# Optimization experiments

Hardware: AMD Instinct MI355X
Metric: run time of the kernel (lower is better)

The kernel has to match this reference:

```python
import jax, jax.numpy as jnp
import numpy as np

TOP_K = 48
NUM_RBF = 16
NUM_RBF_SC = 8
MAXREL = 32
EDGE_F = 128
EPS_D = 1e-6
LN_EPS = 1e-5


def gather_nodes(nodes, idx):
    # nodes: [B, L, C], idx: [B, L, K] -> [B, L, K, C]
    return jax.vmap(lambda n, i: n[i])(nodes, idx)


def rbf(D, count):
    # D: [..., ] -> [..., count]; mu in [2, 22], sigma = 20/count
    mu = jnp.linspace(2.0, 22.0, count)
    sigma = (22.0 - 2.0) / count
    return jnp.exp(-(((D[..., None] - mu) / sigma) ** 2))


def layer_norm(x, g, b):
    mu = jnp.mean(x, -1, keepdims=True)
    var = jnp.mean((x - mu) ** 2, -1, keepdims=True)
    return g * (x - mu) / jnp.sqrt(var + LN_EPS) + b


def setup_inputs() -> dict:
    key = jax.random.key(0)
    ks = jax.random.split(key, 8)
    B, Lr = 1, 1024
    X = jax.random.normal(ks[0], (B, Lr, 37, 3), dtype=jnp.float32)
    mask = jnp.ones((B, Lr), dtype=jnp.float32)
    atom_mask = jnp.ones((B, Lr, 37), dtype=jnp.float32)
    residue_idx = jnp.arange(B * Lr, dtype=jnp.int64 if jax.config.jax_enable_x64 else jnp.int32).reshape(B, Lr)
    dihedral_mask = jnp.ones((B, Lr), dtype=jnp.float32)
    chain_labels = jnp.zeros((B, Lr), dtype=jnp.int32)
    W_pos = jax.random.normal(ks[1], (16, 2 * MAXREL + 2), dtype=jnp.float32) * 0.1
    b_pos = jnp.zeros((16,), dtype=jnp.float32)
    W_e = jax.random.normal(ks[2], (EDGE_F, 16 + NUM_RBF * 25), dtype=jnp.float32) * 0.05
    g_e = jnp.ones((EDGE_F,), dtype=jnp.float32)
    be_e = jnp.zeros((EDGE_F,), dtype=jnp.float32)
    W_s = jax.random.normal(ks[3], (EDGE_F, NUM_RBF_SC * 32 * 5), dtype=jnp.float32) * 0.05
    g_s = jnp.ones((EDGE_F,), dtype=jnp.float32)
    b_s = jnp.zeros((EDGE_F,), dtype=jnp.float32)
    return {"X": X, "L": 1024, "mask": mask, "atom_mask": atom_mask,
            "residue_idx": residue_idx, "dihedral_mask": dihedral_mask,
            "chain_labels": chain_labels, "W_pos": W_pos, "b_pos": b_pos,
            "W_e": W_e, "g_e": g_e, "be_e": be_e, "W_s": W_s, "g_s": g_s, "b_s": b_s}


def reference(X, L, mask, atom_mask, residue_idx, dihedral_mask, chain_labels,
              W_pos, b_pos, W_e, g_e, be_e, W_s, g_s, b_s):
    # Virtual Cb from ideal geometry
    b_v = X[:, :, 1, :] - X[:, :, 0, :]
    c_v = X[:, :, 2, :] - X[:, :, 1, :]
    a_v = jnp.cross(b_v, c_v)
    Cb = -0.58273431 * a_v + 0.56802827 * b_v - 0.54067466 * c_v + X[:, :, 1, :]
    Ca = X[:, :, 1, :]
    N = X[:, :, 0, :]
    C = X[:, :, 2, :]
    O = X[:, :, 4, :]

    # _dist: masked pairwise Ca distances + top-k smallest
    mask2d = mask[:, None, :] * mask[:, :, None]  # [B, L, L]
    dX = Ca[:, :, None, :] - Ca[:, None, :, :]
    D = mask2d * jnp.sqrt(jnp.sum(dX ** 2, -1) + EPS_D)
    D_max = jnp.max(D, -1, keepdims=True)
    D_adj = D + (1.0 - mask2d) * D_max
    neg_vals, E_idx = jax.lax.top_k(-D_adj, TOP_K)
    D_neighbors = -neg_vals  # [B, L, K]

    coords = {'N': N, 'Ca': Ca, 'C': C, 'O': O, 'Cb': Cb}
    pairs = [('N','N'),('C','C'),('O','O'),('Cb','Cb'),('Ca','N'),('Ca','C'),('Ca','O'),
             ('Ca','Cb'),('N','C'),('N','O'),('N','Cb'),('Cb','C'),('Cb','O'),('O','C'),
             ('N','Ca'),('C','Ca'),('O','Ca'),('Cb','Ca'),('C','N'),('O','N'),('Cb','N'),
             ('C','Cb'),('O','Cb'),('C','O')]
    A_st = jnp.stack([coords[a] for a, _ in pairs])  # [24, B, L, 3]
    B_st = jnp.stack([coords[b] for _, b in pairs])
    B_nb = jax.vmap(gather_nodes, (0, None))(B_st, E_idx)  # [24, B, L, K, 3]
    Dp = jnp.sqrt(jnp.sum((A_st[:, :, :, None, :] - B_nb) ** 2, -1) + EPS_D)  # [24,B,L,K]
    RBF_pairs = rbf(Dp, NUM_RBF)  # [24, B, L, K, 16]
    Bt, Lr, K = E_idx.shape
    RBF_pairs = jnp.moveaxis(RBF_pairs, 0, 3).reshape(Bt, Lr, K, 24 * NUM_RBF)
    RBF_all = jnp.concatenate([rbf(D_neighbors, NUM_RBF), RBF_pairs], -1)  # [B,L,K,400]

    # Positional encodings
    ri_nb = gather_nodes(residue_idx[..., None], E_idx)[..., 0]  # [B,L,K]
    offset = residue_idx[:, :, None] - ri_nb
    ch_nb = gather_nodes(chain_labels[..., None], E_idx)[..., 0]
    E_chains = (chain_labels[:, :, None] - ch_nb == 0).astype(jnp.int32)
    d = jnp.clip(offset + MAXREL, 0, 2 * MAXREL) * E_chains + (1 - E_chains) * (2 * MAXREL + 1)
    d_onehot = jax.nn.one_hot(d, 2 * MAXREL + 2, dtype=jnp.float32)
    E_positional = d_onehot @ W_pos.T + b_pos
    E = jnp.concatenate([E_positional, RBF_all], -1)  # [B,L,K,416]

    # Sidechain RBFs on the first min(100, K) neighbors
    Ks = min(100, K)
    E_idx_sub = E_idx[:, :, :Ks]
    am_g = gather_nodes(atom_mask, E_idx_sub)  # [B,L,Ks,37]
    S = X[:, :, 5:37, :]  # [B,L,32,3]
    S_nb = gather_nodes(S.reshape(Bt, Lr, 32 * 3), E_idx_sub).reshape(Bt, Lr, Ks, 32, 3)
    anchors = jnp.stack([N, Ca, C, O, Cb], 2)  # [B,L,5,3], anchor order matches loop order
    Ds = jnp.sqrt(jnp.sum((anchors[:, :, None, :, None, :] - S_nb[:, :, :, None, :, :]) ** 2, -1) + EPS_D)
    # Ds: [B,L,Ks,5,32]; rbf_side -> [B,L,Ks,5,32,8]; masked by neighbor atom mask
    RBF_s = rbf(Ds, NUM_RBF_SC) * am_g[:, :, :, None, 5:37, None]
    E_s = RBF_s.reshape(Bt, Lr, Ks, 5 * 32 * NUM_RBF_SC)  # [B,L,Ks,1280]

    E_s = layer_norm(E_s @ W_s.T, g_s, b_s)
    E = layer_norm(E @ W_e.T, g_e, be_e)
    return (E, E_idx, E_s, E_idx_sub)
```

## Files before the change

### kernel.cpp

```cpp
#include <hip/hip_runtime.h>
#include <math.h>

#define LRES 1024
#define TOPK 48
#define NEDGE (LRES*TOPK)

typedef short short8 __attribute__((ext_vector_type(8)));
typedef float f32x4  __attribute__((ext_vector_type(4)));

#define OUT_E     0
#define OUT_EIDX  6291456
#define OUT_ES    6340608
#define OUT_EIDX2 12632064

#define WS_COORDS 0
#define WS_DNB    15360
#define WS_EIDX   64512
#define WS_WPE    113664
#define WS_WPS    140288

#define DE 1.06666667f
#define QE 0.10273976f
#define DS 1.14285714f
#define QS 0.07337053f

__constant__ int PA[24] = {0,2,3,4,1,1,1,1,0,0,0,4,4,3,0,2,3,4,2,3,4,2,3,2};
__constant__ int PB[24] = {0,2,3,4,0,2,3,4,2,3,4,2,3,2,1,1,1,1,0,0,0,4,4,3};

__device__ inline short f2bf(float f) {
    unsigned u = __float_as_uint(f);
    unsigned r = (u + 0x7FFFu + ((u >> 16) & 1u)) >> 16;
    return (short)r;
}

__device__ inline short8 pack8(const float* fv) {
    union { short8 s; unsigned u[4]; } r;
    #pragma unroll
    for (int i = 0; i < 4; ++i)
        r.u[i] = __builtin_amdgcn_perm(__float_as_uint(fv[2*i+1]),
                                       __float_as_uint(fv[2*i]), 0x07060302u);
    return r.s;
}

__device__ __forceinline__ void kred_ln(const f32x4 (*acc)[8], float* hb,
                                        float* outp, const float* g,
                                        const float* b, int t, int w,
                                        int quad, int l16) {
    int e = t >> 4, c = t & 15;
    float gv[8], bv[8];
    #pragma unroll
    for (int k = 0; k < 8; ++k) { gv[k] = g[c + 16*k]; bv[k] = b[c + 16*k]; }
    float* hw = hb + w*2144;
    #pragma unroll
    for (int mt = 0; mt < 2; ++mt) {
        __syncthreads();
        #pragma unroll
        for (int nt = 0; nt < 8; ++nt)
        #pragma unroll
        for (int r = 0; r < 4; ++r)
            hw[(quad*4 + r)*134 + nt*16 + l16] = acc[mt][nt][r];
        __syncthreads();
        float s = 0.f, s2 = 0.f, vals[8];
        #pragma unroll
        for (int k = 0; k < 8; ++k) {
            int col = e*134 + c + 16*k;
            float v = hb[col] + hb[2144 + col] + hb[4288 + col] + hb[6432 + col];
            vals[k] = v; s += v; s2 = fmaf(v, v, s2);
        }
        #pragma unroll
        for (int m = 1; m <= 8; m <<= 1) {
            s  += __shfl_xor(s,  m);
            s2 += __shfl_xor(s2, m);
        }
        float mu = s * 0.0078125f;
        float rs = rsqrtf(fmaf(s2, 0.0078125f, -mu*mu) + 1e-5f);
        float* row = outp + (size_t)(mt*16 + e)*128 + c;
        #pragma unroll
        for (int k = 0; k < 8; ++k)
            __builtin_nontemporal_store(gv[k]*(vals[k] - mu)*rs + bv[k],
                                        &row[16*k]);
    }
}

__global__ __launch_bounds__(256) void k_pre(const float* __restrict__ X,
                                             const float* __restrict__ mask,
                                             const float* __restrict__ We,
                                             const float* __restrict__ Ws,
                                             float* __restrict__ coords,
                                             short* __restrict__ WpE,
                                             short* __restrict__ WpS,
                                             float* __restrict__ Dnb,
                                             int* __restrict__ Eidx,
                                             float* __restrict__ out) {
    int blk = blockIdx.x, t = threadIdx.x;
    if (blk < 256) {
        __shared__ float sCa[LRES*3];
        __shared__ float sM[LRES];
        for (int j = t; j < LRES; j += 256) {
            sCa[j*3+0] = X[j*111 + 3];
            sCa[j*3+1] = X[j*111 + 4];
            sCa[j*3+2] = X[j*111 + 5];
            sM[j] = mask[j];
        }
        __syncthreads();
        int w = t >> 6, lane = t & 63;
        int i = blk * 4 + w;
        float cx = sCa[i*3], cy = sCa[i*3+1], cz = sCa[i*3+2];
        float mi = sM[i];
        float dv[16], m2v[16];
        float lmax = -1e30f;
        #pragma unroll
        for (int s = 0; s < 16; ++s) {
            int j = s*64 + lane;
            float dx = cx - sCa[j*3], dy = cy - sCa[j*3+1], dz = cz - sCa[j*3+2];
            float d  = __builtin_amdgcn_sqrtf(dx*dx + dy*dy + dz*dz + 1e-6f);
            float m2 = mi * sM[j];
            dv[s] = m2 * d; m2v[s] = m2;
            lmax = fmaxf(lmax, dv[s]);
        }
        #pragma unroll
        for (int off = 32; off; off >>= 1) lmax = fmaxf(lmax, __shfl_xor(lmax, off));
        unsigned long long key[16];
        unsigned long long mkey = ~0ull; int mslot = 0;
        #pragma unroll
        for (int s = 0; s < 16; ++s) {
            float dadj = dv[s] + (1.0f - m2v[s]) * lmax;
            key[s] = (((unsigned long long)__float_as_uint(dadj)) << 10) | (unsigned)(s*64 + lane);
            if (key[s] < mkey) { mkey = key[s]; mslot = s; }
        }
        for (int it = 0; it < TOPK; ++it) {
            unsigned long long wk = mkey;
            #pragma unroll
            for (int off = 32; off; off >>= 1) {
                unsigned long long o = __shfl_xor(wk, off);
                wk = (o < wk) ? o : wk;
            }
            if (lane == 0) {
                int j = (int)(wk & 1023u);
                int id = i*TOPK + it;
                Dnb[id]  = __uint_as_float((unsigned)(wk >> 10));
                Eidx[id] = j;
                out[OUT_EIDX  + id] = (float)j;
                out[OUT_EIDX2 + id] = (float)j;
            }
            if (mkey == wk) {
                key[mslot] = ~0ull;
                mkey = ~0ull;
                #pragma unroll
                for (int s = 0; s < 16; ++s)
                    if (key[s] < mkey) { mkey = key[s]; mslot = s; }
            }
        }
    } else if (blk < 896) {
        int g = (blk - 256) * 256 + t;
        if (g < 8*13*64*8) {
            int j = g & 7, lane = (g >> 3) & 63, gg = g >> 9;
            int ks = gg % 13, nt = gg / 13;
            int n = nt*16 + (lane & 15), k = ks*32 + (lane >> 4)*8 + j;
            WpE[g] = f2bf(We[n*416 + k]);
        }
        if (g < 8*40*64*8) {
            int j = g & 7, lane = (g >> 3) & 63, gg = g >> 9;
            int ks = gg % 40, nt = gg / 40;
            int n = nt*16 + (lane & 15), k = ks*32 + (lane >> 4)*8 + j;
            WpS[g] = f2bf(Ws[n*1280 + k]);
        }
    } else {
        int r = (blk - 896) * 256 + t;
        if (r >= LRES) return;
        const float* xr = X + r * 111;
        float N[3], Ca[3], C[3], O[3], bv[3], cv[3], av[3];
        #pragma unroll
        for (int d = 0; d < 3; ++d) {
            N[d]  = xr[0*3 + d];  Ca[d] = xr[1*3 + d];
            C[d]  = xr[2*3 + d];  O[d]  = xr[4*3 + d];
            bv[d] = Ca[d] - N[d]; cv[d] = C[d] - Ca[d];
        }
        av[0] = bv[1]*cv[2] - bv[2]*cv[1];
        av[1] = bv[2]*cv[0] - bv[0]*cv[2];
        av[2] = bv[0]*cv[1] - bv[1]*cv[0];
        float* o = coords + r * 15;
        #pragma unroll
        for (int d = 0; d < 3; ++d) {
            float Cb = -0.58273431f*av[d] + 0.56802827f*bv[d] - 0.54067466f*cv[d] + Ca[d];
            o[0*3+d] = N[d]; o[1*3+d] = Ca[d]; o[2*3+d] = C[d];
            o[3*3+d] = O[d]; o[4*3+d] = Cb;
        }
    }
}

__global__ __launch_bounds__(256, 2) void k_edge(const float* __restrict__ coords,
                                                 const float* __restrict__ X,
                                                 const float* __restrict__ amask,
                                                 const short* __restrict__ WpE,
                                                 const short* __restrict__ WpS,
                                                 const float* __restrict__ Dnb,
                                                 const int* __restrict__ Eidx,
                                                 const int* __restrict__ ri,
                                                 const int* __restrict__ ch,
                                                 const float* __restrict__ Wpos,
                                                 const float* __restrict__ bpos,
                                                 const float* __restrict__ ge,
                                                 const float* __restrict__ be,
                                                 const float* __restrict__ gs,
                                                 const float* __restrict__ bs,
                                                 float* __restrict__ out) {
    __shared__ float smem[9536];
    int t = threadIdx.x;
    int w = t >> 6, lane = t & 63, quad = lane >> 4, l16 = lane & 15;
    float* hb = smem;

    if (blockIdx.x < 1536) {
        float* sA3 = smem + 8576;
        int id0 = blockIdx.x * 32;
        int i0 = id0 / TOPK;

        if (t < 45) {
            int rr = i0 + t / 15;
            if (rr > LRES-1) rr = LRES-1;
            sA3[t] = coords[rr*15 + t%15];
        }
        int s1 = 4*w + quad;
        float S[2][2][3], am[2][2];
        int im[2];
        #pragma unroll
        for (int mt = 0; mt < 2; ++mt) {
            int id = id0 + mt*16 + l16;
            int j  = Eidx[id];
            im[mt] = id / TOPK;
            const float* xp = X + (j*37 + 5)*3;
            const float* ap = amask + j*37 + 5;
            #pragma unroll
            for (int h = 0; h < 2; ++h) {
                int s = s1 + h*16;
                S[mt][h][0] = xp[s*3+0];
                S[mt][h][1] = xp[s*3+1];
                S[mt][h][2] = xp[s*3+2];
                am[mt][h]   = ap[s];
            }
        }
        __syncthreads();

        f32x4 acc[2][8] = {};
        const short8* bp = (const short8*)WpS;

        for (int a = 0; a < 5; ++a) {
            float A[2][3];
            #pragma unroll
            for (int mt = 0; mt < 2; ++mt) {
                int base = (im[mt] - i0)*15 + a*3;
                A[mt][0] = sA3[base+0];
                A[mt][1] = sA3[base+1];
                A[mt][2] = sA3[base+2];
            }
            #pragma unroll
            for (int h = 0; h < 2; ++h) {
                int ks = a*8 + w + h*4;
                short8 afrag[2];
                #pragma unroll
                for (int mt = 0; mt < 2; ++mt) {
                    float dx = A[mt][0] - S[mt][h][0];
                    float dy = A[mt][1] - S[mt][h][1];
                    float dz = A[mt][2] - S[mt][h][2];
                    float d  = __builtin_amdgcn_sqrtf(fmaf(dz,dz,fmaf(dy,dy,fmaf(dx,dx,1e-6f))));
                    float u  = fmaf(d, 0.4f, -0.8f);
                    float e0 = __expf(-u*u) * am[mt][h];
                    float g  = __expf(fmaf(2.0f*DS, u, -DS*DS));
                    float fv[8];
                    fv[0] = e0;
                    #pragma unroll
                    for (int r = 1; r < 8; ++r) { e0 *= g; g *= QS; fv[r] = e0; }
                    afrag[mt] = pack8(fv);
                }
                #pragma unroll
                for (int nt = 0; nt < 8; ++nt) {
                    short8 b = bp[(nt*40 + ks)*64 + lane];
                    acc[0][nt] = __builtin_amdgcn_mfma_f32_16x16x32_bf16(afrag[0], b, acc[0][nt], 0,0,0);
                    acc[1][nt] = __builtin_amdgcn_mfma_f32_16x16x32_bf16(afrag[1], b, acc[1][nt], 0,0,0);
                }
            }
        }
        kred_ln(acc, hb, out + OUT_ES + (size_t)id0*128, gs, bs, t, w, quad, l16);
    } else {
        float* sA    = smem + 8576;
        float* sB    = smem + 9056;
        float* sdist = hb;
        float* sposf = hb + 864;
        int*   sdpos = (int*)(hb + 1408);
        int id0 = (blockIdx.x - 1536) * 32;

        if (t < 32) {
            int id = id0 + t, i = id / TOPK, j = Eidx[id];
            int off = ri[i] - ri[j];
            sdpos[t] = (ch[i] == ch[j]) ? min(max(off + 32, 0), 64) : 65;
            sdist[t*27] = Dnb[id];
        }
        for (int it = t; it < 32*15; it += 256) {
            int e = it / 15, q = it % 15;
            int id = id0 + e, i = id / TOPK, j = Eidx[id];
            sA[e*15+q] = coords[i*15+q];
            sB[e*15+q] = coords[j*15+q];
        }
        __syncthreads();
        for (int it = t; it < 32*24; it += 256) {
            int e = it / 24, p = it % 24, a = PA[p], b = PB[p];
            float dx = sA[e*15+a*3+0] - sB[e*15+b*3+0];
            float dy = sA[e*15+a*3+1] - sB[e*15+b*3+1];
            float dz = sA[e*15+a*3+2] - sB[e*15+b*3+2];
            sdist[e*27 + 1 + p] = __builtin_amdgcn_sqrtf(dx*dx + dy*dy + dz*dz + 1e-6f);
        }
        for (int it = t; it < 32*16; it += 256) {
            int e = it >> 4, c = it & 15;
            sposf[e*17 + c] = Wpos[c*66 + sdpos[e]] + bpos[c];
        }
        __syncthreads();

        f32x4 acc[2][8] = {};
        const short8* bp = (const short8*)WpE;
        float rb = (quad & 1) ? 8.0f*DE : 0.0f;

        for (int ks = w; ks < 13; ks += 4) {
            short8 afrag[2];
            #pragma unroll
            for (int mt = 0; mt < 2; ++mt) {
                int e = mt*16 + l16;
                float fv[8];
                if (ks == 0 && quad < 2) {
                    #pragma unroll
                    for (int j = 0; j < 8; ++j) fv[j] = sposf[e*17 + quad*8 + j];
                } else {
                    int p = (ks == 0) ? 0 : (2*ks - 1 + (quad >> 1));
                    float d = sdist[e*27 + p];
                    float u = fmaf(d, 0.8f, -1.6f) - rb;
                    float e0 = __expf(-u*u);
                    float g  = __expf(fmaf(2.0f*DE, u, -DE*DE));
                    fv[0] = e0;
                    #pragma unroll
                    for (int r = 1; r < 8; ++r) { e0 *= g; g *= QE; fv[r] = e0; }
                }
                afrag[mt] = pack8(fv);
            }
            #pragma unroll
            for (int nt = 0; nt < 8; ++nt) {
                short8 b = bp[(nt*13 + ks)*64 + lane];
                acc[0][nt] = __builtin_amdgcn_mfma_f32_16x16x32_bf16(afrag[0], b, acc[0][nt], 0,0,0);
                acc[1][nt] = __builtin_amdgcn_mfma_f32_16x16x32_bf16(afrag[1], b, acc[1][nt], 0,0,0);
            }
        }
        kred_ln(acc, hb, out + OUT_E + (size_t)id0*128, ge, be, t, w, quad, l16);
    }
}

extern "C" void kernel_launch(void* const* d_in, const int* in_sizes, int n_in,
                              void* d_out, int out_size, void* d_ws, size_t ws_size,
                              hipStream_t stream) {
    (void)in_sizes; (void)n_in; (void)out_size; (void)ws_size;
    const float* X     = (const float*)d_in[0];
    const float* mask  = (const float*)d_in[2];
    const float* amask = (const float*)d_in[3];
    const int*   ri    = (const int*)d_in[4];
    const int*   ch    = (const int*)d_in[6];
    const float* Wpos  = (const float*)d_in[7];
    const float* bpos  = (const float*)d_in[8];
    const float* We    = (const float*)d_in[9];
    const float* ge    = (const float*)d_in[10];
    const float* be    = (const float*)d_in[11];
    const float* Ws    = (const float*)d_in[12];
    const float* gs    = (const float*)d_in[13];
    const float* bs    = (const float*)d_in[14];

    float* out    = (float*)d_out;
    float* ws     = (float*)d_ws;
    float* coords = ws + WS_COORDS;
    float* Dnb    = ws + WS_DNB;
    int*   Eidx   = (int*)(ws + WS_EIDX);
    short* WpE    = (short*)(ws + WS_WPE);
    short* WpS    = (short*)(ws + WS_WPS);

    k_pre <<<dim3(900),  dim3(256), 0, stream>>>(X, mask, We, Ws, coords,
                                                 WpE, WpS, Dnb, Eidx, out);
    k_edge<<<dim3(3072), dim3(256), 0, stream>>>(coords, X, amask, WpE, WpS,
                                                 Dnb, Eidx, ri, ch, Wpos, bpos,
                                                 ge, be, gs, bs, out);
}
```

Measured before the change: 182.9 us.

## Halve LDS reduction buffer and interleave sidechain and edge blocks

The cross-wave reduction before layernorm now stages half of the N tiles at a time, which shrinks the shared buffer from about 37KB to about 19KB per block. The cost is two extra barrier pairs per M tile. Block indexing is also changed so even blocks do sidechain work and odd blocks do edge work on the same 32-edge chunk. The aim is higher LDS-limited occupancy and a better mix of the two workloads across CUs, at the price of more synchronisation.

After: 188.9 us. 3.3% more time.

```diff
diff --git a/kernel.cpp b/kernel.cpp
--- a/kernel.cpp
+++ b/kernel.cpp
@@ -23,6 +23,9 @@
 #define QE 0.10273976f
 #define DS 1.14285714f
 #define QS 0.07337053f
+
+#define HBR 74
+#define HBW 1186
 
 __constant__ int PA[24] = {0,2,3,4,1,1,1,1,0,0,0,4,4,3,0,2,3,4,2,3,4,2,3,2};
 __constant__ int PB[24] = {0,2,3,4,0,2,3,4,2,3,4,2,3,2,1,1,1,1,0,0,0,4,4,3};
@@ -50,22 +53,25 @@
     float gv[8], bv[8];
     #pragma unroll
     for (int k = 0; k < 8; ++k) { gv[k] = g[c + 16*k]; bv[k] = b[c + 16*k]; }
-    float* hw = hb + w*2144;
+    float* hw = hb + w*HBW;
     #pragma unroll
     for (int mt = 0; mt < 2; ++mt) {
-        __syncthreads();
-        #pragma unroll
-        for (int nt = 0; nt < 8; ++nt)
-        #pragma unroll
-        for (int r = 0; r < 4; ++r)
-            hw[(quad*4 + r)*134 + nt*16 + l16] = acc[mt][nt][r];
-        __syncthreads();
         float s = 0.f, s2 = 0.f, vals[8];
         #pragma unroll
-        for (int k = 0; k < 8; ++k) {
-            int col = e*134 + c + 16*k;
-            float v = hb[col] + hb[2144 + col] + hb[4288 + col] + hb[6432 + col];
-            vals[k] = v; s += v; s2 = fmaf(v, v, s2);
+        for (int nh = 0; nh < 2; ++nh) {
+            __syncthreads();
+            #pragma unroll
+            for (int ntp = 0; ntp < 4; ++ntp)
+            #pragma unroll
+            for (int r = 0; r < 4; ++r)
+                hw[(quad*4 + r)*HBR + ntp*16 + l16] = acc[mt][nh*4 + ntp][r];
+            __syncthreads();
+            #pragma unroll
+            for (int kp = 0; kp < 4; ++kp) {
+                int col = e*HBR + c + 16*kp;
+                float v = hb[col] + hb[HBW + col] + hb[2*HBW + col] + hb[3*HBW + col];
+                vals[nh*4 + kp] = v; s += v; s2 = fmaf(v, v, s2);
+            }
         }
         #pragma unroll
         for (int m = 1; m <= 8; m <<= 1) {
@@ -205,14 +211,14 @@
                                                  const float* __restrict__ gs,
                                                  const float* __restrict__ bs,
                                                  float* __restrict__ out) {
-    __shared__ float smem[9536];
+    __shared__ float smem[4*HBW + 48];
     int t = threadIdx.x;
     int w = t >> 6, lane = t & 63, quad = lane >> 4, l16 = lane & 15;
     float* hb = smem;
-
-    if (blockIdx.x < 1536) {
-        float* sA3 = smem + 8576;
-        int id0 = blockIdx.x * 32;
+    int id0 = (blockIdx.x >> 1) * 32;
+
+    if (!(blockIdx.x & 1)) {
+        float* sA3 = smem + 4*HBW;
         int i0 = id0 / TOPK;
 
         if (t < 45) {
@@ -282,12 +288,11 @@
         }
         kred_ln(acc, hb, out + OUT_ES + (size_t)id0*128, gs, bs, t, w, quad, l16);
     } else {
-        float* sA    = smem + 8576;
-        float* sB    = smem + 9056;
         float* sdist = hb;
         float* sposf = hb + 864;
         int*   sdpos = (int*)(hb + 1408);
-        int id0 = (blockIdx.x - 1536) * 32;
+        float* sA    = hb + 1440;
+        float* sB    = hb + 1920;
 
         if (t < 32) {
             int id = id0 + t, i = id / TOPK, j = Eidx[id];
```
